# Kernel tuning notes

Hardware: AMD Instinct MI355X
Metric: run time of the kernel (lower is better)

The kernel has to match this reference:

```python
import jax, jax.numpy as jnp
import numpy as np

B, T, H, NSPK = 8, 1024, 1024, 2
LN_EPS = 1e-5


def setup_inputs() -> dict:
    key = jax.random.key(0)
    ks = jax.random.split(key, 12)
    s = 1.0 / np.sqrt(H)
    return {
        "x": jax.random.normal(ks[0], (B, T, H), jnp.float32),
        "qmask": jax.random.uniform(ks[1], (B, T, NSPK), jnp.float32),
        "dia_len": jax.random.randint(ks[2], (B,), T // 2, T + 1),
        "wp": 8,
        "wf": 8,
        "W_msg": jax.random.normal(ks[3], (H, H), jnp.float32) * s,
        "b_msg": jax.random.normal(ks[4], (H,), jnp.float32) * s,
        "W_self": jax.random.normal(ks[5], (H, H), jnp.float32) * s,
        "b_self": jax.random.normal(ks[6], (H,), jnp.float32) * s,
        "W_out": jax.random.normal(ks[7], (H, H), jnp.float32) * s,
        "b_out": jax.random.normal(ks[8], (H,), jnp.float32) * s,
        "gamma": jnp.ones((H,), jnp.float32),
        "beta": jnp.zeros((H,), jnp.float32),
    }


def reference(x, qmask, dia_len, wp, wf, W_msg, b_msg, W_self, b_self, W_out, b_out, gamma, beta):
    Bb, Tt, Hh = x.shape
    spk = jnp.argmax(qmask, axis=-1)                     # [B,T]
    pos = jnp.arange(Tt)
    offs = jnp.arange(-wp, wf + 1)                       # [W]
    idx = pos[:, None] + offs[None, :]                   # [T,W] window indices
    vlen = dia_len[:, None, None]                        # [B,1,1]
    valid = (idx[None] >= 0) & (idx[None] <= vlen - 1)   # [B,T,W]
    idxc = jnp.clip(idx, 0, Tt - 1)
    nb = jnp.take(x, idxc, axis=1)                       # [B,T,W,H]
    nb_spk = jnp.take(spk, idxc, axis=1)                 # [B,T,W]
    same = (nb_spk == spk[:, :, None]).astype(x.dtype)
    w = jnp.where(valid, 0.5 + 0.5 * same, 0.0)          # speaker weights, masked
    cnt = jnp.maximum(valid.sum(-1).astype(x.dtype), 1.0)  # window sizes [B,T]
    msg = jnp.einsum('btw,btwh->bth', w, nb) / cnt[..., None]
    h = x @ W_self + b_self + msg @ W_msg + b_msg        # per-node fusion
    node_valid = (pos[None, :] < dia_len[:, None])[..., None]
    out = jnp.where(node_valid, h, x)                    # nodes past dia_len keep x
    y = jax.nn.relu(out) @ W_out + b_out                 # dropout = identity (eval)
    z = x + y
    mean = z.mean(-1, keepdims=True)
    var = z.var(-1, keepdims=True)
    return gamma * (z - mean) / jnp.sqrt(var + LN_EPS) + beta
```

## Files before the change

### kernel.cpp

```cpp
#include <hip/hip_runtime.h>


typedef unsigned short u16;
typedef float floatx4 __attribute__((ext_vector_type(4)));
typedef short shortx8 __attribute__((ext_vector_type(8)));

#define T_ 1024
#define H_ 1024

__device__ __forceinline__ float bf2f(u16 v) {
    return __uint_as_float(((unsigned)v) << 16);
}
__device__ __forceinline__ u16 f2bf(float f) {
    unsigned u = __float_as_uint(f);
    return (u16)((u + 0x7fffu + ((u >> 16) & 1u)) >> 16);
}
__device__ __forceinline__ void async16(const void* g, void* l) {
    __builtin_amdgcn_global_load_lds(
        (__attribute__((address_space(1))) void*)g,
        (__attribute__((address_space(3))) void*)l, 16, 0, 0);
}

__global__ __launch_bounds__(256)
void pack_x(const float* __restrict__ x, u16* __restrict__ xbf)
{
    const size_t i = ((size_t)blockIdx.x * 256 + threadIdx.x) * 4;
    float4 v = *(const float4*)(x + i);
    ushort4 o;
    o.x = f2bf(v.x); o.y = f2bf(v.y); o.z = f2bf(v.z); o.w = f2bf(v.w);
    *(ushort4*)(xbf + i) = o;
}

__global__ __launch_bounds__(256)
void transpose_pack(const float* __restrict__ Wself, const float* __restrict__ Wmsg,
                    const float* __restrict__ Wout,
                    u16* __restrict__ wt1, u16* __restrict__ wt_out)
{
    __shared__ float s[32][33];
    const int wid = blockIdx.z;
    const float* src = (wid == 0) ? Wself : ((wid == 1) ? Wmsg : Wout);
    const int n0 = blockIdx.x * 32, k0 = blockIdx.y * 32;
    const int tx = threadIdx.x & 31, ty = threadIdx.x >> 5;
#pragma unroll
    for (int i = 0; i < 4; ++i) {
        int k = k0 + ty + 8 * i;
        s[ty + 8 * i][tx] = src[(size_t)k * H_ + n0 + tx];
    }
    __syncthreads();
#pragma unroll
    for (int i = 0; i < 4; ++i) {
        int n = n0 + ty + 8 * i;
        u16 v = f2bf(s[tx][ty + 8 * i]);
        if (wid == 0)      wt1[(size_t)n * 1024 + k0 + tx] = v;
        else if (wid == 1) wt1[(size_t)(n + 1024) * 1024 + k0 + tx] = v;
        else               wt_out[(size_t)n * 1024 + k0 + tx] = v;
    }
}

template <int KLEN, int EPI>
__global__ __launch_bounds__(256)
void gemm_bt(const u16* __restrict__ A, const u16* __restrict__ Bt,
             u16* __restrict__ O0, u16* __restrict__ O1)
{
    __shared__ u16 sA[128 * 32];
    __shared__ u16 sB[128 * 32];
    const int tid = threadIdx.x;
    const int bn = blockIdx.x * 128;
    const int bm = blockIdx.y * 128;
    const int kb = blockIdx.z * KLEN;
    const int wave = tid >> 6, lane = tid & 63;
    const int wr = wave >> 1, wc = wave & 1;
    const int lrow = lane & 15, lq = lane >> 4;

    const u16* gA0 = A + (size_t)(bm + (tid >> 2)) * 1024 + kb + (tid & 3) * 8;
    const u16* gA1 = gA0 + (size_t)64 * 1024;
    const u16* gB0 = Bt + (size_t)(bn + (tid >> 2)) * 1024 + kb + (tid & 3) * 8;
    const u16* gB1 = gB0 + (size_t)64 * 1024;
    u16* lA = sA + wave * 512;
    u16* lB = sB + wave * 512;

    floatx4 acc[4][4];
#pragma unroll
    for (int i = 0; i < 4; ++i)
#pragma unroll
        for (int j = 0; j < 4; ++j)
            acc[i][j] = (floatx4){0.f, 0.f, 0.f, 0.f};

    const u16* pa = sA + (wr * 64 + lrow) * 32 + lq * 8;
    const u16* pb = sB + (wc * 64 + lrow) * 32 + lq * 8;

    for (int k0 = 0; k0 < KLEN; k0 += 32) {
        __syncthreads();
        async16(gA0 + k0, lA);
        async16(gA1 + k0, lA + 2048);
        async16(gB0 + k0, lB);
        async16(gB1 + k0, lB + 2048);
        __syncthreads();
        shortx8 av[4], bv[4];
#pragma unroll
        for (int i = 0; i < 4; ++i) av[i] = *(const shortx8*)(pa + i * 512);
#pragma unroll
        for (int j = 0; j < 4; ++j) bv[j] = *(const shortx8*)(pb + j * 512);
#pragma unroll
        for (int i = 0; i < 4; ++i)
#pragma unroll
            for (int j = 0; j < 4; ++j)
                acc[i][j] = __builtin_amdgcn_mfma_f32_16x16x32_bf16(
                    av[i], bv[j], acc[i][j], 0, 0, 0);
    }

    u16* O;
    int cbase;
    if (EPI == 0) { O = (bn < 1024) ? O0 : O1; cbase = bn & 1023; }
    else          { O = blockIdx.z ? O1 : O0;  cbase = bn; }
#pragma unroll
    for (int i = 0; i < 4; ++i) {
        const int row0 = bm + wr * 64 + i * 16 + lq * 4;
#pragma unroll
        for (int j = 0; j < 4; ++j) {
            const int col = cbase + wc * 64 + j * 16 + lrow;
#pragma unroll
            for (int r = 0; r < 4; ++r)
                O[(size_t)(row0 + r) * 1024 + col] = f2bf(acc[i][j][r]);
        }
    }
}

__global__ __launch_bounds__(256)
void combine(const u16* __restrict__ u, const u16* __restrict__ v,
             const float* __restrict__ x, const float* __restrict__ qmask,
             const int* __restrict__ dia_len, const float* __restrict__ b_self,
             const float* __restrict__ b_msg, u16* __restrict__ r)
{
    __shared__ u16 sv[32][1024];
    const int tid = threadIdx.x;
    const int b = blockIdx.y;
    const int t0 = blockIdx.x * 16;
    const int dlen = dia_len[b];
    const int c4 = tid * 4;

    unsigned spkmask = 0;
#pragma unroll 4
    for (int rr = 0; rr < 32; ++rr) {
        int row = t0 - 8 + rr;
        row = row < 0 ? 0 : (row > T_ - 1 ? T_ - 1 : row);
        const float* q = qmask + ((size_t)b * T_ + row) * 2;
        spkmask |= (q[1] > q[0] ? 1u : 0u) << rr;
        *(ushort4*)&sv[rr][c4] =
            *(const ushort4*)(v + ((size_t)b * T_ + row) * 1024 + c4);
    }
    __syncthreads();

    float4 bs;
    {
        float4 b1 = *(const float4*)(b_self + c4);
        float4 b2 = *(const float4*)(b_msg + c4);
        bs.x = b1.x + b2.x; bs.y = b1.y + b2.y;
        bs.z = b1.z + b2.z; bs.w = b1.w + b2.w;
    }

    for (int lt = 0; lt < 16; ++lt) {
        const int t = t0 + lt;
        const unsigned cs = (spkmask >> (lt + 8)) & 1u;
        float a0 = 0.f, a1 = 0.f, a2 = 0.f, a3 = 0.f;
        int cnt = 0;
#pragma unroll
        for (int o = 0; o < 17; ++o) {
            const int idx = t + o - 8;
            if (idx >= 0 && idx < dlen) {
                const float w = (((spkmask >> (lt + o)) & 1u) == cs) ? 1.0f : 0.5f;
                ++cnt;
                ushort4 uu = *(const ushort4*)&sv[lt + o][c4];
                a0 += w * bf2f(uu.x); a1 += w * bf2f(uu.y);
                a2 += w * bf2f(uu.z); a3 += w * bf2f(uu.w);
            }
        }
        const float inv = 1.0f / (float)(cnt > 0 ? cnt : 1);
        const size_t rowg = (size_t)b * T_ + t;
        ushort4 u4 = *(const ushort4*)(u + rowg * 1024 + c4);
        float4 xv = *(const float4*)(x + rowg * H_ + c4);
        const bool sel = (t < dlen);
        float h0 = bf2f(u4.x) + bs.x + a0 * inv;
        float h1 = bf2f(u4.y) + bs.y + a1 * inv;
        float h2 = bf2f(u4.z) + bs.z + a2 * inv;
        float h3 = bf2f(u4.w) + bs.w + a3 * inv;
        ushort4 out;
        out.x = f2bf(fmaxf(sel ? h0 : xv.x, 0.f));
        out.y = f2bf(fmaxf(sel ? h1 : xv.y, 0.f));
        out.z = f2bf(fmaxf(sel ? h2 : xv.z, 0.f));
        out.w = f2bf(fmaxf(sel ? h3 : xv.w, 0.f));
        *(ushort4*)(r + rowg * 1024 + c4) = out;
    }
}

__global__ __launch_bounds__(256)
void ln_final(const u16* __restrict__ P0, const u16* __restrict__ P1,
              const float* __restrict__ x, const float* __restrict__ b_out,
              const float* __restrict__ gamma, const float* __restrict__ beta,
              float* __restrict__ out)
{
    const int row = blockIdx.x;
    const int tid = threadIdx.x;
    const size_t base = (size_t)row * H_ + tid * 4;
    float4 xv = *(const float4*)(x + base);
    ushort4 p0 = *(const ushort4*)(P0 + base);
    ushort4 p1 = *(const ushort4*)(P1 + base);
    float4 bo = *(const float4*)(b_out + tid * 4);
    float4 v;
    v.x = xv.x + bf2f(p0.x) + bf2f(p1.x) + bo.x;
    v.y = xv.y + bf2f(p0.y) + bf2f(p1.y) + bo.y;
    v.z = xv.z + bf2f(p0.z) + bf2f(p1.z) + bo.z;
    v.w = xv.w + bf2f(p0.w) + bf2f(p1.w) + bo.w;
    float s = v.x + v.y + v.z + v.w;
    float q = v.x * v.x + v.y * v.y + v.z * v.z + v.w * v.w;
#pragma unroll
    for (int off = 32; off > 0; off >>= 1) {
        s += __shfl_down(s, off);
        q += __shfl_down(q, off);
    }
    __shared__ float ps[4], pq[4];
    const int wave = tid >> 6, lane = tid & 63;
    if (lane == 0) { ps[wave] = s; pq[wave] = q; }
    __syncthreads();
    const float S = ps[0] + ps[1] + ps[2] + ps[3];
    const float Q = pq[0] + pq[1] + pq[2] + pq[3];
    const float mean = S * (1.0f / 1024.0f);
    const float var = Q * (1.0f / 1024.0f) - mean * mean;
    const float inv = rsqrtf(var + 1e-5f);
    float4 g = *(const float4*)(gamma + tid * 4);
    float4 bt = *(const float4*)(beta + tid * 4);
    float4 o;
    o.x = g.x * (v.x - mean) * inv + bt.x;
    o.y = g.y * (v.y - mean) * inv + bt.y;
    o.z = g.z * (v.z - mean) * inv + bt.z;
    o.w = g.w * (v.w - mean) * inv + bt.w;
    *(float4*)(out + base) = o;
}

extern "C" void kernel_launch(void* const* d_in, const int* in_sizes, int n_in,
                              void* d_out, int out_size, void* d_ws, size_t ws_size,
                              hipStream_t stream)
{
    (void)in_sizes; (void)n_in; (void)out_size; (void)ws_size;
    const float* x       = (const float*)d_in[0];
    const float* qmask   = (const float*)d_in[1];
    const int*   dia_len = (const int*)d_in[2];
    const float* W_msg   = (const float*)d_in[5];
    const float* b_msg   = (const float*)d_in[6];
    const float* W_self  = (const float*)d_in[7];
    const float* b_self  = (const float*)d_in[8];
    const float* W_out   = (const float*)d_in[9];
    const float* b_out   = (const float*)d_in[10];
    const float* gamma   = (const float*)d_in[11];
    const float* beta    = (const float*)d_in[12];
    float* out = (float*)d_out;

    char* ws = (char*)d_ws;
    u16* region0 = (u16*)ws;
    u16* region1 = (u16*)(ws + (size_t)(16u << 20));
    u16* region2 = (u16*)(ws + (size_t)(32u << 20));
    u16* wt1     = (u16*)(ws + (size_t)(48u << 20));
    u16* wt_out  = (u16*)(ws + (size_t)(52u << 20));

    pack_x<<<dim3(8192), 256, 0, stream>>>(x, region0);
    transpose_pack<<<dim3(32, 32, 3), 256, 0, stream>>>(W_self, W_msg, W_out,
                                                        wt1, wt_out);
    gemm_bt<1024, 0><<<dim3(16, 64, 1), 256, 0, stream>>>(region0, wt1,
                                                          region1, region2);
    combine<<<dim3(64, 8), 256, 0, stream>>>(region1, region2, x, qmask,
                                             dia_len, b_self, b_msg, region0);
    gemm_bt<512, 1><<<dim3(8, 64, 2), 256, 0, stream>>>(region0, wt_out,
                                                        region1, region2);
    ln_final<<<dim3(8192), 256, 0, stream>>>(region1, region2, x, b_out,
                                             gamma, beta, out);
}
```

Before: 238.9 us.

## Double-buffer LDS tiles in bf16 GEMM and compute combine in place

The GEMM kernel now uses two LDS stages. It issues the async global-to-LDS loads for the next K-slice before computing the current one, and waits with an explicit vmcnt and raw s_barrier instead of two __syncthreads per step. This aims to overlap load latency with MFMA work. The combine kernel now writes its result over the u buffer, and the buffer assignments for the later kernels are remapped to match. The LDS footprint per block doubles, which may reduce occupancy.

```diff
diff --git a/kernel.cpp b/kernel.cpp
--- a/kernel.cpp
+++ b/kernel.cpp
@@ -62,8 +62,7 @@
 void gemm_bt(const u16* __restrict__ A, const u16* __restrict__ Bt,
              u16* __restrict__ O0, u16* __restrict__ O1)
 {
-    __shared__ u16 sA[128 * 32];
-    __shared__ u16 sB[128 * 32];
+    __shared__ u16 smem[2 * 8192];
     const int tid = threadIdx.x;
     const int bn = blockIdx.x * 128;
     const int bm = blockIdx.y * 128;
@@ -76,8 +75,6 @@
     const u16* gA1 = gA0 + (size_t)64 * 1024;
     const u16* gB0 = Bt + (size_t)(bn + (tid >> 2)) * 1024 + kb + (tid & 3) * 8;
     const u16* gB1 = gB0 + (size_t)64 * 1024;
-    u16* lA = sA + wave * 512;
-    u16* lB = sB + wave * 512;
 
     floatx4 acc[4][4];
 #pragma unroll
@@ -86,16 +83,32 @@
         for (int j = 0; j < 4; ++j)
             acc[i][j] = (floatx4){0.f, 0.f, 0.f, 0.f};
 
-    const u16* pa = sA + (wr * 64 + lrow) * 32 + lq * 8;
-    const u16* pb = sB + (wc * 64 + lrow) * 32 + lq * 8;
-
-    for (int k0 = 0; k0 < KLEN; k0 += 32) {
-        __syncthreads();
-        async16(gA0 + k0, lA);
-        async16(gA1 + k0, lA + 2048);
-        async16(gB0 + k0, lB);
-        async16(gB1 + k0, lB + 2048);
-        __syncthreads();
+    const int aoff = (wr * 64 + lrow) * 32 + lq * 8;
+    const int boff = 4096 + (wc * 64 + lrow) * 32 + lq * 8;
+
+    auto issue = [&](int s, int p) {
+        u16* base = smem + p * 8192 + wave * 512;
+        const int k = s * 32;
+        async16(gA0 + k, base);
+        async16(gA1 + k, base + 2048);
+        async16(gB0 + k, base + 4096);
+        async16(gB1 + k, base + 4096 + 2048);
+    };
+
+    constexpr int NS = KLEN / 32;
+    issue(0, 0);
+#pragma unroll 2
+    for (int s = 0; s < NS; ++s) {
+        const int p = s & 1;
+        if (s + 1 < NS) {
+            issue(s + 1, p ^ 1);
+            asm volatile("s_waitcnt vmcnt(4)" ::: "memory");
+        } else {
+            asm volatile("s_waitcnt vmcnt(0)" ::: "memory");
+        }
+        asm volatile("s_barrier" ::: "memory");
+        const u16* pa = smem + p * 8192 + aoff;
+        const u16* pb = smem + p * 8192 + boff;
         shortx8 av[4], bv[4];
 #pragma unroll
         for (int i = 0; i < 4; ++i) av[i] = *(const shortx8*)(pa + i * 512);
@@ -107,6 +120,7 @@
             for (int j = 0; j < 4; ++j)
                 acc[i][j] = __builtin_amdgcn_mfma_f32_16x16x32_bf16(
                     av[i], bv[j], acc[i][j], 0, 0, 0);
+        asm volatile("s_barrier" ::: "memory");
     }
 
     u16* O;
@@ -127,10 +141,10 @@
 }
 
 __global__ __launch_bounds__(256)
-void combine(const u16* __restrict__ u, const u16* __restrict__ v,
+void combine(u16* uv, const u16* __restrict__ v,
              const float* __restrict__ x, const float* __restrict__ qmask,
              const int* __restrict__ dia_len, const float* __restrict__ b_self,
-             const float* __restrict__ b_msg, u16* __restrict__ r)
+             const float* __restrict__ b_msg)
 {
     __shared__ u16 sv[32][1024];
     const int tid = threadIdx.x;
@@ -177,19 +191,19 @@
         }
         const float inv = 1.0f / (float)(cnt > 0 ? cnt : 1);
         const size_t rowg = (size_t)b * T_ + t;
-        ushort4 u4 = *(const ushort4*)(u + rowg * 1024 + c4);
+        ushort4 u4 = *(const ushort4*)(uv + rowg * 1024 + c4);
         float4 xv = *(const float4*)(x + rowg * H_ + c4);
         const bool sel = (t < dlen);
         float h0 = bf2f(u4.x) + bs.x + a0 * inv;
         float h1 = bf2f(u4.y) + bs.y + a1 * inv;
         float h2 = bf2f(u4.z) + bs.z + a2 * inv;
         float h3 = bf2f(u4.w) + bs.w + a3 * inv;
-        ushort4 out;
-        out.x = f2bf(fmaxf(sel ? h0 : xv.x, 0.f));
-        out.y = f2bf(fmaxf(sel ? h1 : xv.y, 0.f));
-        out.z = f2bf(fmaxf(sel ? h2 : xv.z, 0.f));
-        out.w = f2bf(fmaxf(sel ? h3 : xv.w, 0.f));
-        *(ushort4*)(r + rowg * 1024 + c4) = out;
+        ushort4 outv;
+        outv.x = f2bf(fmaxf(sel ? h0 : xv.x, 0.f));
+        outv.y = f2bf(fmaxf(sel ? h1 : xv.y, 0.f));
+        outv.z = f2bf(fmaxf(sel ? h2 : xv.z, 0.f));
+        outv.w = f2bf(fmaxf(sel ? h3 : xv.w, 0.f));
+        *(ushort4*)(uv + rowg * 1024 + c4) = outv;
     }
 }
 
@@ -268,9 +282,9 @@
     gemm_bt<1024, 0><<<dim3(16, 64, 1), 256, 0, stream>>>(region0, wt1,
                                                           region1, region2);
     combine<<<dim3(64, 8), 256, 0, stream>>>(region1, region2, x, qmask,
-                                             dia_len, b_self, b_msg, region0);
-    gemm_bt<512, 1><<<dim3(8, 64, 2), 256, 0, stream>>>(region0, wt_out,
-                                                        region1, region2);
-    ln_final<<<dim3(8192), 256, 0, stream>>>(region1, region2, x, b_out,
+                                             dia_len, b_self, b_msg);
+    gemm_bt<512, 1><<<dim3(8, 64, 2), 256, 0, stream>>>(region1, wt_out,
+                                                        region2, region0);
+    ln_final<<<dim3(8192), 256, 0, stream>>>(region2, region0, x, b_out,
                                              gamma, beta, out);
 }
```

Measured after the change: 234.5 us. Within noise of the previous version (-1.9%).
